# Kernel optimization log

Hardware: AMD Instinct MI355X
Metric: run time of the kernel (lower is better)

Reference implementation:

```python
import jax, jax.numpy as jnp
import numpy as np

N, T, D, H, DA = 128, 256, 512, 512, 4


def setup_inputs() -> dict:
    key = jax.random.key(0)
    k1, k2, k3, k4, k5, k6 = jax.random.split(key, 6)
    x = jax.random.normal(k1, (N, T, D), dtype=jnp.float32)
    A = jax.random.normal(k2, (N, H, DA, DA), dtype=jnp.float32)
    Wx = jax.random.normal(k3, (D, 4 * H), dtype=jnp.float32) / np.sqrt(D).astype(np.float32)
    Wh = jax.random.normal(k4, (H, 4 * H), dtype=jnp.float32) / np.sqrt(H).astype(np.float32)
    Wattn = jax.random.normal(k5, (H, 4 * H), dtype=jnp.float32) / np.sqrt(H).astype(np.float32)
    b = jnp.zeros((4 * H,), dtype=jnp.float32)
    return {"x": x, "A": A, "Wx": Wx, "Wh": Wh, "Wattn": Wattn, "b": b}


def _attn(prev_h, A_flat, scale):
    # prev_h: (N,H), A_flat: (N,H,P) with P = DA*DA
    scores = jnp.einsum('nh,nhp->np', prev_h, A_flat) * scale      # (N,P)
    w = jax.nn.softmax(scores, axis=-1)                             # (N,P)
    attn = jnp.einsum('nhp,np->nh', A_flat, w)                      # (N,H)
    return attn


def reference(x, A, Wx, Wh, Wattn, b):
    n, t, d = x.shape
    h_dim = A.shape[1]
    scale = 1.0 / jnp.sqrt(jnp.asarray(h_dim, dtype=x.dtype))
    A_flat = A.reshape(n, h_dim, -1)
    h0 = jnp.mean(A, axis=(2, 3))  # (N,H)
    c0 = h0
    xs = jnp.moveaxis(x, 1, 0)     # (T,N,D)

    def step(carry, x_t):
        prev_h, prev_c = carry
        attn = _attn(prev_h, A_flat, scale)
        a = x_t @ Wx + prev_h @ Wh + attn @ Wattn + b  # (N,4H)
        i, f, o, g = jnp.split(a, 4, axis=-1)
        next_c = jax.nn.sigmoid(f) * prev_c + jax.nn.sigmoid(i) * jnp.tanh(g)
        next_h = jax.nn.sigmoid(o) * jnp.tanh(next_c)
        return (next_h, next_c), next_h

    _, hs = jax.lax.scan(step, (h0, c0), xs)  # hs: (T,N,H)
    return jnp.moveaxis(hs, 0, 1)             # (N,T,H)
```

## Files before the change

kernel.cpp:

```cpp
#include <hip/hip_runtime.h>
#include <hip/hip_bf16.h>

typedef __bf16 bf16_t;
typedef __bf16 bf16x8 __attribute__((ext_vector_type(8)));
typedef float  f32x4  __attribute__((ext_vector_type(4)));

#define N_    128
#define T_    256
#define D_    512
#define H_    512
#define G4    2048
#define ZB_ELEMS 131072
#define WB_PER_CB 32768

__device__ __forceinline__ int zidx(int k, int n) {
  return ((((k >> 5) * 8 + (n >> 4)) * 64) + ((k >> 3) & 3) * 16 + (n & 15)) * 8 + (k & 7);
}

__device__ __forceinline__ float sigf(float x) { return 1.f / (1.f + __expf(-x)); }
__device__ __forceinline__ float tanhfast(float x) {
  float e = __expf(2.f * x);
  return 1.f - 2.f / (e + 1.f);
}

__device__ __forceinline__ bf16x8 ld_frag_llc(const bf16_t* p) {
  unsigned long long lo = __hip_atomic_load((const unsigned long long*)p,
      __ATOMIC_RELAXED, __HIP_MEMORY_SCOPE_AGENT);
  unsigned long long hi = __hip_atomic_load(((const unsigned long long*)p) + 1,
      __ATOMIC_RELAXED, __HIP_MEMORY_SCOPE_AGENT);
  union { unsigned long long q[2]; bf16x8 v; } u; u.q[0] = lo; u.q[1] = hi; return u.v;
}
__device__ __forceinline__ float ld_f32_llc(const float* p) {
  return __hip_atomic_load(p, __ATOMIC_RELAXED, __HIP_MEMORY_SCOPE_AGENT);
}
__device__ __forceinline__ void st_u32_llc(unsigned int* p, unsigned int v) {
  __hip_atomic_store(p, v, __ATOMIC_RELAXED, __HIP_MEMORY_SCOPE_AGENT);
}
__device__ __forceinline__ int ld_i32_llc(const int* p) {
  return __hip_atomic_load(p, __ATOMIC_RELAXED, __HIP_MEMORY_SCOPE_AGENT);
}
__device__ __forceinline__ unsigned int pack2bf(float lo, float hi) {
  union { bf16_t h[2]; unsigned int u; } q;
  q.h[0] = (bf16_t)lo; q.h[1] = (bf16_t)hi; return q.u;
}

__global__ void prepW_kernel(const float* __restrict__ Wh, const float* __restrict__ Wx,
                             bf16_t* __restrict__ Wb) {
  int cb = blockIdx.x >> 1, kq = blockIdx.x & 1;
  int tt = threadIdx.x;
  int hl = tt & 7, gate = (tt >> 3) & 3, ko = tt >> 5;
  int oc = gate * H_ + cb * 8 + hl;
  int jpl = hl * 4 + gate;
  int wcl = jpl >> 4, c = jpl & 15;
  for (int kb = kq * 64; kb < kq * 64 + 64; kb++) {
    int k = kb * 8 + ko;
    float v = (k < 512) ? Wh[(size_t)k * G4 + oc] : Wx[(size_t)(k - 512) * G4 + oc];
    int kk = k >> 5, ch = (k >> 3) & 3, e = k & 7;
    Wb[(size_t)cb * WB_PER_CB + (((kk * 2 + wcl) * 64) + ch * 16 + c) * 8 + e] = (bf16_t)v;
  }
}

__global__ void prepA_kernel(const float* __restrict__ A, const float* __restrict__ x,
                             bf16_t* __restrict__ A_sc, float* __restrict__ cbuf,
                             bf16_t* __restrict__ Zb, float* __restrict__ S,
                             int* __restrict__ bar) {
  __shared__ float a_ld[8192];
  __shared__ float h0s[512];
  __shared__ float redb[256 * 16];
  int n = blockIdx.x, tid = threadIdx.x;
  if (n == 0 && tid < 144) bar[tid * 32] = 0;
  if (tid < 16) S[2048 + n * 16 + tid] = 0.f;
  for (int i = tid; i < 8192; i += 256) a_ld[i] = A[(size_t)n * 8192 + i];
  __syncthreads();
  for (int h = tid; h < H_; h += 256) {
    float s = 0.f;
#pragma unroll
    for (int p = 0; p < 16; p++) s += a_ld[h * 16 + p];
    s *= (1.f / 16.f);
    h0s[h] = s;
    cbuf[n * H_ + h] = s;
    Zb[zidx(h, n)] = (bf16_t)s;
  }
  for (int d = tid; d < D_; d += 256)
    Zb[zidx(512 + d, n)] = (bf16_t)x[(size_t)n * T_ * D_ + d];
  for (int idx = tid; idx < 8192; idx += 256) {
    int k = idx >> 4, p = idx & 15;
    A_sc[(size_t)n * 8192 + ((k >> 3) * 16 + p) * 8 + (k & 7)] = (bf16_t)a_ld[idx];
  }
  __syncthreads();
  float part[16];
#pragma unroll
  for (int p = 0; p < 16; p++) part[p] = 0.f;
  for (int h = tid; h < H_; h += 256) {
    float hv = h0s[h];
#pragma unroll
    for (int p = 0; p < 16; p++) part[p] += hv * a_ld[h * 16 + p];
  }
#pragma unroll
  for (int p = 0; p < 16; p++) redb[tid * 16 + p] = part[p];
  __syncthreads();
  if (tid < 16) {
    float s = 0.f;
    for (int i = 0; i < 256; i++) s += redb[i * 16 + tid];
    S[n * 16 + tid] = s;
  }
}

__global__ void __launch_bounds__(256) prepB_kernel(const float* __restrict__ Wattn,
                             const bf16_t* __restrict__ A_sc, bf16_t* __restrict__ Bg) {
  __shared__ bf16_t Al[8192];
  int n = blockIdx.x >> 2, jpQ = blockIdx.x & 3;
  int tid = threadIdx.x, p = tid & 15, jg = tid >> 4;
  for (int i = tid; i < 1024; i += 256)
    ((bf16x8*)Al)[i] = ((const bf16x8*)(A_sc + (size_t)n * 8192))[i];
  __syncthreads();
  int cbb = jpQ * 16 + jg;
  float acc[32];
#pragma unroll
  for (int j = 0; j < 32; j++) acc[j] = 0.f;
  for (int k = 0; k < 512; k++) {
    float a = (float)Al[((k >> 3) * 16 + p) * 8 + (k & 7)];
    const float* wr = Wattn + (size_t)k * G4 + cbb * 8;
#pragma unroll
    for (int gate = 0; gate < 4; gate++) {
      const float4* w4 = (const float4*)(wr + gate * H_);
      float4 wa = w4[0], wb = w4[1];
      acc[0 * 4 + gate] += a * wa.x; acc[1 * 4 + gate] += a * wa.y;
      acc[2 * 4 + gate] += a * wa.z; acc[3 * 4 + gate] += a * wa.w;
      acc[4 * 4 + gate] += a * wb.x; acc[5 * 4 + gate] += a * wb.y;
      acc[6 * 4 + gate] += a * wb.z; acc[7 * 4 + gate] += a * wb.w;
    }
  }
  bf16_t* dst = Bg + (((size_t)n * 64 + cbb) * 32) * 16 + p;
#pragma unroll
  for (int jj = 0; jj < 32; jj++) dst[jj * 16] = (bf16_t)acc[jj];
}

__device__ __forceinline__ void gridbar(int* gbase, int leaf, int g0r, int g0l) {
  __syncthreads();
  if (threadIdx.x == 0) {
    int* leafctr  = gbase + leaf * 32;
    int* rootctr  = gbase + 8 * 32;
    int* gen_root = gbase + 9 * 32;
    int* gen_leaf = gbase + (10 + leaf) * 32;
    int my = __hip_atomic_fetch_add(leafctr, 1, __ATOMIC_RELAXED, __HIP_MEMORY_SCOPE_AGENT);
    if ((my & 7) == 7) {
      int r = __hip_atomic_fetch_add(rootctr, 1, __ATOMIC_RELAXED, __HIP_MEMORY_SCOPE_AGENT);
      if ((r & 7) == 7) {
        __hip_atomic_fetch_add(gen_root, 1, __ATOMIC_RELAXED, __HIP_MEMORY_SCOPE_AGENT);
      } else {
        while (ld_i32_llc(gen_root) == g0r) __builtin_amdgcn_s_sleep(2);
      }
      __hip_atomic_fetch_add(gen_leaf, 1, __ATOMIC_RELAXED, __HIP_MEMORY_SCOPE_AGENT);
    } else {
      while (ld_i32_llc(gen_leaf) == g0l) __builtin_amdgcn_s_sleep(2);
    }
  }
  __syncthreads();
}

__global__ void __launch_bounds__(256, 2)
lstm_kernel(const float* __restrict__ x, const bf16_t* __restrict__ A_sc,
            const bf16_t* __restrict__ Wb, const bf16_t* __restrict__ Bg,
            const float* __restrict__ bvec, const float* __restrict__ cbuf,
            bf16_t* __restrict__ Zb, float* __restrict__ S,
            float* __restrict__ out, int* __restrict__ bar) {
  __shared__ bf16_t Wl[32768];
  __shared__ f32x4 red[2][64];
  __shared__ float hsh[16 * 9];
  __shared__ float wls[16 * 17];

  const int wg = blockIdx.x, tid = threadIdx.x;
  const int cb = wg & 63, grp = wg >> 6;
  const int wave = tid >> 6, lane = tid & 63;
  const int wc = wave & 1, kh = wave >> 1;
  const int nb = grp;
  const int s  = grp * 16 + (lane & 15);
  const int hc = cb * 8 + wc * 4 + (lane >> 4);
  const int jp = cb * 32 + wc * 16 + (lane & 15);
  const float bias_l = bvec[(jp & 3) * H_ + (jp >> 2)];
  const int jl = wc * 16 + (lane & 15);
  const int leaf = cb >> 3;
  int* gbase = bar + grp * 18 * 32;

  {
    const bf16x8* src = (const bf16x8*)(Wb + (size_t)cb * WB_PER_CB);
    bf16x8* dst = (bf16x8*)Wl;
    for (int i = tid; i < 4096; i += 256) dst[i] = src[i];
  }
  float creg = cbuf[s * H_ + hc];
  __syncthreads();

  int cur = 0;
  for (int t = 0; t < T_; t++) {
    const bf16_t* Zc = Zb + cur * ZB_ELEMS;
    bf16_t* Zn = Zb + (cur ^ 1) * ZB_ELEMS;
    const int cur3 = t % 3, nxt3 = (t + 1) % 3, z3 = (t + 2) % 3;

    int g0r = 0, g0l = 0;
    if (tid == 0) {
      g0r = ld_i32_llc(gbase + 9 * 32);
      g0l = ld_i32_llc(gbase + (10 + leaf) * 32);
    }
    asm volatile("" ::: "memory");

    if (tid < 4) st_u32_llc((unsigned int*)(S + z3 * 2048 + grp * 256 + cb * 4 + tid), 0u);

    if (t + 1 < T_ && tid < 64) {
      int nl = tid >> 2, e2 = (tid & 3) * 2;
      int n = grp * 16 + nl;
      const float* xp = x + ((size_t)n * T_ + (t + 1)) * D_ + cb * 8 + e2;
      st_u32_llc((unsigned int*)(Zn + zidx(512 + cb * 8 + e2, n)), pack2bf(xp[0], xp[1]));
    }

    if ((tid & 63) < 4) {
      int nl = wave * 4 + (tid & 63);
      int ng = grp * 16 + nl;
      float r[16];
#pragma unroll
      for (int p = 0; p < 16; p++)
        r[p] = ld_f32_llc(S + cur3 * 2048 + ng * 16 + p) * 0.044194173824159216f;
      float m = r[0];
#pragma unroll
      for (int p = 1; p < 16; p++) m = fmaxf(m, r[p]);
      float ssum = 0.f;
#pragma unroll
      for (int p = 0; p < 16; p++) { r[p] = __expf(r[p] - m); ssum += r[p]; }
      float inv = 1.f / ssum;
#pragma unroll
      for (int p = 0; p < 16; p++) wls[nl * 17 + p] = r[p] * inv;
    }

    f32x4 acc = {0.f, 0.f, 0.f, 0.f};
    {
      const bf16x8* Wf = (const bf16x8*)Wl;
#pragma unroll 8
      for (int i = 0; i < 16; i++) {
        int kk = kh * 16 + i;
        bf16x8 a = ld_frag_llc(Zc + ((size_t)(kk * 8 + nb) * 64 + lane) * 8);
        bf16x8 b = Wf[(kk * 2 + wc) * 64 + lane];
        acc = __builtin_amdgcn_mfma_f32_16x16x32_bf16(a, b, acc, 0, 0, 0);
      }
    }
    if (kh == 1) red[wc][lane] = acc;
    __syncthreads();

    if (kh == 0) {
      {
        f32x4 o = red[wc][lane];
        acc[0] += o[0]; acc[1] += o[1]; acc[2] += o[2]; acc[3] += o[3];
      }
      const int nl0 = (lane >> 4) << 2;
#pragma unroll
      for (int rp = 0; rp < 4; rp++) {
        int nl = nl0 + rp;
        const bf16x8* bl = (const bf16x8*)(Bg +
            (((size_t)(grp * 16 + nl) * 64 + cb) * 32 + jl) * 16);
        bf16x8 b0 = bl[0], b1 = bl[1];
        const float* wn = wls + nl * 17;
        float add = 0.f;
#pragma unroll
        for (int p = 0; p < 8; p++) add += wn[p] * (float)b0[p];
#pragma unroll
        for (int p = 0; p < 8; p++) add += wn[8 + p] * (float)b1[p];
        acc[rp] += add + bias_l;
      }

      float gv[4] = {0.f, 0.f, 0.f, 0.f};
      const int srcbase = ((lane >> 2) & 3) * 16 + (lane >> 4) * 4;
#pragma unroll
      for (int rp = 0; rp < 4; rp++) {
        float v = acc[rp];
#pragma unroll
        for (int g = 0; g < 4; g++) {
          float sv = __shfl(v, srcbase + g, 64);
          if ((lane & 3) == rp) gv[g] = sv;
        }
      }

      float si = sigf(gv[0]), sf = sigf(gv[1]), so = sigf(gv[2]);
      float cn = sf * creg + si * tanhfast(gv[3]);
      float hn = so * tanhfast(cn);
      creg = cn;
      __builtin_nontemporal_store(hn, out + ((size_t)s * T_ + t) * H_ + hc);

      union { bf16_t h; unsigned short u; } cvt; cvt.h = (bf16_t)hn;
      unsigned int hbits = cvt.u;
      unsigned int other = __shfl(hbits, (lane + 16) & 63, 64);
      if (((lane >> 4) & 1) == 0)
        st_u32_llc((unsigned int*)(Zn + zidx(hc, s)), hbits | (other << 16));
      hsh[(s & 15) * 9 + (hc & 7)] = hn;
    }
    __syncthreads();

    if (t + 1 < T_) {
      int nl = tid >> 4, p = tid & 15;
      int ng = grp * 16 + nl;
      const bf16x8 av = *(const bf16x8*)(A_sc + ((size_t)ng * 64 + cb) * 128 + p * 8);
      float part = 0.f;
#pragma unroll
      for (int c = 0; c < 8; c++) part += hsh[nl * 9 + c] * (float)av[c];
      atomicAdd(S + nxt3 * 2048 + ng * 16 + p, part);
    }

    gridbar(gbase, leaf, g0r, g0l);
    cur ^= 1;
  }
}

extern "C" void kernel_launch(void* const* d_in, const int* in_sizes, int n_in,
                              void* d_out, int out_size, void* d_ws, size_t ws_size,
                              hipStream_t stream) {
  const float* x     = (const float*)d_in[0];
  const float* A     = (const float*)d_in[1];
  const float* Wx    = (const float*)d_in[2];
  const float* Wh    = (const float*)d_in[3];
  const float* Wattn = (const float*)d_in[4];
  const float* bv    = (const float*)d_in[5];
  float* out = (float*)d_out;

  char* ws = (char*)d_ws;
  const size_t BAR_OFF = 0;
  const size_t S_OFF   = 32768;
  const size_t CB_OFF  = 57344;
  const size_t ZB_OFF  = 319488;
  const size_t ASC_OFF = 843776;
  const size_t WB_OFF  = 2940928;
  const size_t BG_OFF  = 7135232;
  const size_t WS_NEED = 15523840;
  if (ws_size < WS_NEED) return;

  int*    bar  = (int*)(ws + BAR_OFF);
  float*  S    = (float*)(ws + S_OFF);
  float*  cbuf = (float*)(ws + CB_OFF);
  bf16_t* Zb   = (bf16_t*)(ws + ZB_OFF);
  bf16_t* A_sc = (bf16_t*)(ws + ASC_OFF);
  bf16_t* Wb   = (bf16_t*)(ws + WB_OFF);
  bf16_t* Bg   = (bf16_t*)(ws + BG_OFF);

  prepW_kernel<<<dim3(128), dim3(256), 0, stream>>>(Wh, Wx, Wb);
  prepA_kernel<<<dim3(128), dim3(256), 0, stream>>>(A, x, A_sc, cbuf, Zb, S, bar);
  prepB_kernel<<<dim3(512), dim3(256), 0, stream>>>(Wattn, A_sc, Bg);
  lstm_kernel<<<dim3(512), dim3(256), 0, stream>>>(x, A_sc, Wb, Bg, bv, cbuf, Zb, S, out, bar);
}
```

Baseline: 2.286 ms.

## Precompute bf16 x fragments, split K across four waves, simplify grid barrier

Adds a prep kernel that converts all x timesteps into MFMA-fragment bf16 layout up front, so the recurrent kernel no longer writes x into the shared Z buffer each step. Waves 2-3 then read their x fragments with plain loads and do not wait on coherent LLC loads. All four waves now each cover a quarter of K for both column halves, with a 4-way LDS reduction, and all fragment loads are hoisted before the softmax work. The grid barrier is reworked so the root winner writes every leaf generation flag directly instead of using a two-level generation scheme. In exchange it needs about 33 MB more workspace and falls back to the old path if that space is not available.

```diff
diff --git a/kernel.cpp b/kernel.cpp
--- a/kernel.cpp
+++ b/kernel.cpp
@@ -11,6 +11,7 @@
 #define H_    512
 #define G4    2048
 #define ZB_ELEMS 131072
+#define XF_PER_T 65536
 #define WB_PER_CB 32768
 
 __device__ __forceinline__ int zidx(int k, int n) {
@@ -60,6 +61,20 @@
   }
 }
 
+__global__ void prepX_kernel(const float* __restrict__ x, bf16_t* __restrict__ Xf) {
+  int gid = blockIdx.x * 256 + threadIdx.x;
+  int e8 = gid & 63;
+  int n  = (gid >> 6) & 127;
+  int t  = gid >> 13;
+  int k  = e8 * 8;
+  const float* xp = x + ((size_t)n * T_ + t) * D_ + k;
+  union { bf16_t b[8]; bf16x8 v; } u;
+#pragma unroll
+  for (int e = 0; e < 8; e++) u.b[e] = (bf16_t)xp[e];
+  int idx = ((k >> 5) * 8 + (n >> 4)) * 64 + ((k >> 3) & 3) * 16 + (n & 15);
+  ((bf16x8*)(Xf + (size_t)t * XF_PER_T))[idx] = u.v;
+}
+
 __global__ void prepA_kernel(const float* __restrict__ A, const float* __restrict__ x,
                              bf16_t* __restrict__ A_sc, float* __restrict__ cbuf,
                              bf16_t* __restrict__ Zb, float* __restrict__ S,
@@ -136,59 +151,58 @@
   for (int jj = 0; jj < 32; jj++) dst[jj * 16] = (bf16_t)acc[jj];
 }
 
-__device__ __forceinline__ void gridbar(int* gbase, int leaf, int g0r, int g0l) {
+__device__ __forceinline__ void gridbar(int* gbase, int leaf, int g0l) {
   __syncthreads();
   if (threadIdx.x == 0) {
-    int* leafctr  = gbase + leaf * 32;
-    int* rootctr  = gbase + 8 * 32;
-    int* gen_root = gbase + 9 * 32;
-    int* gen_leaf = gbase + (10 + leaf) * 32;
-    int my = __hip_atomic_fetch_add(leafctr, 1, __ATOMIC_RELAXED, __HIP_MEMORY_SCOPE_AGENT);
+    int my = __hip_atomic_fetch_add(gbase + leaf * 32, 1, __ATOMIC_RELAXED, __HIP_MEMORY_SCOPE_AGENT);
+    bool rootwin = false;
     if ((my & 7) == 7) {
-      int r = __hip_atomic_fetch_add(rootctr, 1, __ATOMIC_RELAXED, __HIP_MEMORY_SCOPE_AGENT);
+      int r = __hip_atomic_fetch_add(gbase + 8 * 32, 1, __ATOMIC_RELAXED, __HIP_MEMORY_SCOPE_AGENT);
       if ((r & 7) == 7) {
-        __hip_atomic_fetch_add(gen_root, 1, __ATOMIC_RELAXED, __HIP_MEMORY_SCOPE_AGENT);
-      } else {
-        while (ld_i32_llc(gen_root) == g0r) __builtin_amdgcn_s_sleep(2);
-      }
-      __hip_atomic_fetch_add(gen_leaf, 1, __ATOMIC_RELAXED, __HIP_MEMORY_SCOPE_AGENT);
-    } else {
-      while (ld_i32_llc(gen_leaf) == g0l) __builtin_amdgcn_s_sleep(2);
-    }
-  }
-  __syncthreads();
-}
-
+        rootwin = true;
+#pragma unroll
+        for (int l = 0; l < 8; l++)
+          st_u32_llc((unsigned int*)(gbase + (9 + l) * 32), (unsigned int)(g0l + 1));
+      }
+    }
+    if (!rootwin) {
+      while (ld_i32_llc(gbase + (9 + leaf) * 32) == g0l) __builtin_amdgcn_s_sleep(1);
+    }
+  }
+  __syncthreads();
+}
+
+template<int USE_XF>
 __global__ void __launch_bounds__(256, 2)
-lstm_kernel(const float* __restrict__ x, const bf16_t* __restrict__ A_sc,
+lstm_kernel(const bf16_t* __restrict__ Xf, const bf16_t* __restrict__ A_sc,
             const bf16_t* __restrict__ Wb, const bf16_t* __restrict__ Bg,
             const float* __restrict__ bvec, const float* __restrict__ cbuf,
             bf16_t* __restrict__ Zb, float* __restrict__ S,
-            float* __restrict__ out, int* __restrict__ bar) {
+            float* __restrict__ out, int* __restrict__ bar,
+            const float* __restrict__ x) {
   __shared__ bf16_t Wl[32768];
-  __shared__ f32x4 red[2][64];
+  __shared__ f32x4 red[4][2][64];
   __shared__ float hsh[16 * 9];
   __shared__ float wls[16 * 17];
 
   const int wg = blockIdx.x, tid = threadIdx.x;
   const int cb = wg & 63, grp = wg >> 6;
   const int wave = tid >> 6, lane = tid & 63;
-  const int wc = wave & 1, kh = wave >> 1;
-  const int nb = grp;
   const int s  = grp * 16 + (lane & 15);
-  const int hc = cb * 8 + wc * 4 + (lane >> 4);
-  const int jp = cb * 32 + wc * 16 + (lane & 15);
-  const float bias_l = bvec[(jp & 3) * H_ + (jp >> 2)];
-  const int jl = wc * 16 + (lane & 15);
+  const int hcE = cb * 8 + wave * 4 + (lane >> 4);
+  const int jpE = cb * 32 + wave * 16 + (lane & 15);
+  const float bias_l = (wave < 2) ? bvec[(jpE & 3) * H_ + (jpE >> 2)] : 0.f;
+  const int jl = wave * 16 + (lane & 15);
   const int leaf = cb >> 3;
   int* gbase = bar + grp * 18 * 32;
+  const int kkb = wave * 8;
 
   {
     const bf16x8* src = (const bf16x8*)(Wb + (size_t)cb * WB_PER_CB);
     bf16x8* dst = (bf16x8*)Wl;
     for (int i = tid; i < 4096; i += 256) dst[i] = src[i];
   }
-  float creg = cbuf[s * H_ + hc];
+  float creg = (wave < 2) ? cbuf[s * H_ + hcE] : 0.f;
   __syncthreads();
 
   int cur = 0;
@@ -197,22 +211,31 @@
     bf16_t* Zn = Zb + (cur ^ 1) * ZB_ELEMS;
     const int cur3 = t % 3, nxt3 = (t + 1) % 3, z3 = (t + 2) % 3;
 
-    int g0r = 0, g0l = 0;
-    if (tid == 0) {
-      g0r = ld_i32_llc(gbase + 9 * 32);
-      g0l = ld_i32_llc(gbase + (10 + leaf) * 32);
-    }
+    int g0l = 0;
+    if (tid == 0) g0l = ld_i32_llc(gbase + (9 + leaf) * 32);
     asm volatile("" ::: "memory");
 
     if (tid < 4) st_u32_llc((unsigned int*)(S + z3 * 2048 + grp * 256 + cb * 4 + tid), 0u);
 
-    if (t + 1 < T_ && tid < 64) {
+    if (!USE_XF && t + 1 < T_ && tid < 64) {
       int nl = tid >> 2, e2 = (tid & 3) * 2;
       int n = grp * 16 + nl;
       const float* xp = x + ((size_t)n * T_ + (t + 1)) * D_ + cb * 8 + e2;
       st_u32_llc((unsigned int*)(Zn + zidx(512 + cb * 8 + e2, n)), pack2bf(xp[0], xp[1]));
     }
 
+    bf16x8 afrag[8];
+    if (USE_XF && wave >= 2) {
+      const bf16x8* xf = (const bf16x8*)(Xf + (size_t)t * XF_PER_T);
+#pragma unroll
+      for (int i = 0; i < 8; i++)
+        afrag[i] = xf[((kkb - 16 + i) * 8 + grp) * 64 + lane];
+    } else {
+#pragma unroll
+      for (int i = 0; i < 8; i++)
+        afrag[i] = ld_frag_llc(Zc + ((size_t)((kkb + i) * 8 + grp) * 64 + lane) * 8);
+    }
+
     if ((tid & 63) < 4) {
       int nl = wave * 4 + (tid & 63);
       int ng = grp * 16 + nl;
@@ -231,24 +254,26 @@
       for (int p = 0; p < 16; p++) wls[nl * 17 + p] = r[p] * inv;
     }
 
-    f32x4 acc = {0.f, 0.f, 0.f, 0.f};
+    f32x4 acc0 = {0.f, 0.f, 0.f, 0.f}, acc1 = {0.f, 0.f, 0.f, 0.f};
     {
       const bf16x8* Wf = (const bf16x8*)Wl;
-#pragma unroll 8
-      for (int i = 0; i < 16; i++) {
-        int kk = kh * 16 + i;
-        bf16x8 a = ld_frag_llc(Zc + ((size_t)(kk * 8 + nb) * 64 + lane) * 8);
-        bf16x8 b = Wf[(kk * 2 + wc) * 64 + lane];
-        acc = __builtin_amdgcn_mfma_f32_16x16x32_bf16(a, b, acc, 0, 0, 0);
-      }
-    }
-    if (kh == 1) red[wc][lane] = acc;
+#pragma unroll
+      for (int i = 0; i < 8; i++) {
+        int kk = kkb + i;
+        acc0 = __builtin_amdgcn_mfma_f32_16x16x32_bf16(afrag[i], Wf[(kk * 2 + 0) * 64 + lane], acc0, 0, 0, 0);
+        acc1 = __builtin_amdgcn_mfma_f32_16x16x32_bf16(afrag[i], Wf[(kk * 2 + 1) * 64 + lane], acc1, 0, 0, 0);
+      }
+    }
+    red[wave][0][lane] = acc0;
+    red[wave][1][lane] = acc1;
     __syncthreads();
 
-    if (kh == 0) {
-      {
-        f32x4 o = red[wc][lane];
-        acc[0] += o[0]; acc[1] += o[1]; acc[2] += o[2]; acc[3] += o[3];
+    if (wave < 2) {
+      f32x4 fa = red[0][wave][lane];
+#pragma unroll
+      for (int w = 1; w < 4; w++) {
+        f32x4 o = red[w][wave][lane];
+        fa[0] += o[0]; fa[1] += o[1]; fa[2] += o[2]; fa[3] += o[3];
       }
       const int nl0 = (lane >> 4) << 2;
 #pragma unroll
@@ -263,14 +288,14 @@
         for (int p = 0; p < 8; p++) add += wn[p] * (float)b0[p];
 #pragma unroll
         for (int p = 0; p < 8; p++) add += wn[8 + p] * (float)b1[p];
-        acc[rp] += add + bias_l;
+        fa[rp] += add + bias_l;
       }
 
       float gv[4] = {0.f, 0.f, 0.f, 0.f};
       const int srcbase = ((lane >> 2) & 3) * 16 + (lane >> 4) * 4;
 #pragma unroll
       for (int rp = 0; rp < 4; rp++) {
-        float v = acc[rp];
+        float v = fa[rp];
 #pragma unroll
         for (int g = 0; g < 4; g++) {
           float sv = __shfl(v, srcbase + g, 64);
@@ -282,14 +307,14 @@
       float cn = sf * creg + si * tanhfast(gv[3]);
       float hn = so * tanhfast(cn);
       creg = cn;
-      __builtin_nontemporal_store(hn, out + ((size_t)s * T_ + t) * H_ + hc);
+      __builtin_nontemporal_store(hn, out + ((size_t)s * T_ + t) * H_ + hcE);
 
       union { bf16_t h; unsigned short u; } cvt; cvt.h = (bf16_t)hn;
       unsigned int hbits = cvt.u;
       unsigned int other = __shfl(hbits, (lane + 16) & 63, 64);
       if (((lane >> 4) & 1) == 0)
-        st_u32_llc((unsigned int*)(Zn + zidx(hc, s)), hbits | (other << 16));
-      hsh[(s & 15) * 9 + (hc & 7)] = hn;
+        st_u32_llc((unsigned int*)(Zn + zidx(hcE, s)), hbits | (other << 16));
+      hsh[(s & 15) * 9 + (hcE & 7)] = hn;
     }
     __syncthreads();
 
@@ -303,7 +328,7 @@
       atomicAdd(S + nxt3 * 2048 + ng * 16 + p, part);
     }
 
-    gridbar(gbase, leaf, g0r, g0l);
+    gridbar(gbase, leaf, g0l);
     cur ^= 1;
   }
 }
@@ -327,8 +352,11 @@
   const size_t ASC_OFF = 843776;
   const size_t WB_OFF  = 2940928;
   const size_t BG_OFF  = 7135232;
-  const size_t WS_NEED = 15523840;
-  if (ws_size < WS_NEED) return;
+  const size_t XF_OFF  = 15523840;
+  const size_t WS_BASE = 15523840;
+  const size_t WS_XF   = 49078272;
+  if (ws_size < WS_BASE) return;
+  const bool use_xf = (ws_size >= WS_XF);
 
   int*    bar  = (int*)(ws + BAR_OFF);
   float*  S    = (float*)(ws + S_OFF);
@@ -337,9 +365,15 @@
   bf16_t* A_sc = (bf16_t*)(ws + ASC_OFF);
   bf16_t* Wb   = (bf16_t*)(ws + WB_OFF);
   bf16_t* Bg   = (bf16_t*)(ws + BG_OFF);
+  bf16_t* Xf   = (bf16_t*)(ws + XF_OFF);
 
   prepW_kernel<<<dim3(128), dim3(256), 0, stream>>>(Wh, Wx, Wb);
   prepA_kernel<<<dim3(128), dim3(256), 0, stream>>>(A, x, A_sc, cbuf, Zb, S, bar);
   prepB_kernel<<<dim3(512), dim3(256), 0, stream>>>(Wattn, A_sc, Bg);
-  lstm_kernel<<<dim3(512), dim3(256), 0, stream>>>(x, A_sc, Wb, Bg, bv, cbuf, Zb, S, out, bar);
-}
+  if (use_xf) {
+    prepX_kernel<<<dim3(8192), dim3(256), 0, stream>>>(x, Xf);
+    lstm_kernel<1><<<dim3(512), dim3(256), 0, stream>>>(Xf, A_sc, Wb, Bg, bv, cbuf, Zb, S, out, bar, x);
+  } else {
+    lstm_kernel<0><<<dim3(512), dim3(256), 0, stream>>>(Xf, A_sc, Wb, Bg, bv, cbuf, Zb, S, out, bar, x);
+  }
+}
```

Result: faster. 1.946 ms (-14.9%).
